# Optimization experiments

Measured on AMD Instinct MI355X. Metric: run time of the kernel, lower is better.

The kernel has to match this reference:

```python
import jax, jax.numpy as jnp
import numpy as np

B, S, V, E, H = 2048, 128, 128, 300, 512  # batch, max_length, vocab, embed, hidden (enc_outstate_dim == H)


def setup_inputs() -> dict:
    key = jax.random.key(0)
    ks = jax.random.split(key, 20)
    s = 0.05
    return {
        "x": jax.random.randint(ks[0], (B, 1), 0, V),
        "hidden": jax.random.normal(ks[1], (1, B, H), jnp.float32),
        "enc_output": jax.random.normal(ks[2], (B, S, H), jnp.float32),
        "emb_table": jax.random.normal(ks[3], (V, E), jnp.float32) * s,
        "W1_w": jax.random.normal(ks[4], (H, H), jnp.float32) * s,
        "W1_b": jnp.zeros((H,), jnp.float32),
        "W2_w": jax.random.normal(ks[5], (H, H), jnp.float32) * s,
        "W2_b": jnp.zeros((H,), jnp.float32),
        "V_w": jax.random.normal(ks[6], (1, H), jnp.float32) * s,
        "V_b": jnp.zeros((1,), jnp.float32),
        "gru_w_ih": jax.random.normal(ks[7], (3 * H, E + H), jnp.float32) * s,
        "gru_w_hh": jax.random.normal(ks[8], (3 * H, H), jnp.float32) * s,
        "gru_b_ih": jnp.zeros((3 * H,), jnp.float32),
        "gru_b_hh": jnp.zeros((3 * H,), jnp.float32),
        "fc1_w": jax.random.normal(ks[9], (E, H), jnp.float32) * s,
        "fc1_b": jnp.zeros((E,), jnp.float32),
        "fc2_w": jax.random.normal(ks[10], (V, E), jnp.float32) * s,
        "fc2_b": jnp.zeros((V,), jnp.float32),
    }


def reference(x, hidden, enc_output, emb_table, W1_w, W1_b, W2_w, W2_b, V_w, V_b,
              gru_w_ih, gru_w_hh, gru_b_ih, gru_b_hh, fc1_w, fc1_b, fc2_w, fc2_b):
    emb = emb_table[x[:, 0]]  # [B,E]
    # Bahdanau additive attention
    hsum = jnp.sum(hidden, axis=0)  # [B,H] (sum over layers)
    score = jnp.tanh(enc_output @ W1_w.T + W1_b + (hsum @ W2_w.T + W2_b)[:, None, :])  # [B,S,H]
    attw = jax.nn.softmax(score @ V_w.T + V_b, axis=1)  # [B,S,1]
    ctx = jnp.sum(attw * enc_output, axis=1)  # [B,H]
    # single-step GRU (PyTorch gate layout: r,z,n)
    gin = jnp.concatenate([ctx, emb], axis=-1)  # [B,H+E]
    h0 = hidden[0]
    gi = gin @ gru_w_ih.T + gru_b_ih
    gh = h0 @ gru_w_hh.T + gru_b_hh
    i_r, i_z, i_n = gi[:, :H], gi[:, H:2 * H], gi[:, 2 * H:]
    h_r, h_z, h_n = gh[:, :H], gh[:, H:2 * H], gh[:, 2 * H:]
    r = jax.nn.sigmoid(i_r + h_r)
    z = jax.nn.sigmoid(i_z + h_z)
    n = jnp.tanh(i_n + r * h_n)
    h_new = (1.0 - z) * n + z * h0  # [B,H]
    # FC head
    y = jax.nn.leaky_relu(h_new @ fc1_w.T + fc1_b, 0.01) @ fc2_w.T + fc2_b  # [B,V]
    return y, h_new[None]
```

## Files before the change

kernel.cpp:

```cpp
#include <hip/hip_runtime.h>


typedef __attribute__((ext_vector_type(4))) float floatx4;
typedef __attribute__((ext_vector_type(8))) short short8;
typedef unsigned short us;

#define DEV static __device__ __forceinline__

DEV us f2bf(float f) {
  unsigned u = __float_as_uint(f);
  u = u + 0x7fffu + ((u >> 16) & 1u);
  return (us)(u >> 16);
}
DEV float bf2f(us s) { return __uint_as_float(((unsigned)s) << 16); }
DEV float tanh_fast(float x) {
  float e = __expf(2.f * x);
  return 1.f - 2.f / (e + 1.f);
}
DEV float sigmoid_fast(float x) { return 1.f / (1.f + __expf(-x)); }
DEV unsigned pack2(float a, float b) {
  return (unsigned)f2bf(a) | ((unsigned)f2bf(b) << 16);
}

#define S0 262144
#define S1 1310720
#define S2 2588672
#define S3 2785280
#define S4 2834432
#define S5 3883008
#define S6 3885056
#define S7 3885440
#define S8 4540800

__global__ void prep_kernel(const float* __restrict__ W1w,
                            const float* __restrict__ W2w,
                            const float* __restrict__ whh,
                            const float* __restrict__ wih,
                            const float* __restrict__ fc1w,
                            const float* __restrict__ fc2w,
                            const float* __restrict__ hidden,
                            const float* __restrict__ W1b,
                            const float* __restrict__ W2b,
                            const float* __restrict__ bhh,
                            const float* __restrict__ fc1b,
                            const int* __restrict__ x,
                            const float* __restrict__ embt,
                            us* __restrict__ W1bf, us* __restrict__ wcomb,
                            us* __restrict__ wihbf, us* __restrict__ fc1wbf,
                            us* __restrict__ fc2wbf, us* __restrict__ hidbf,
                            float* __restrict__ bcomb,
                            float* __restrict__ fc1bp,
                            us* __restrict__ ginbf) {
  int idx = blockIdx.x * 256 + threadIdx.x;
  if (idx < S0) {
    W1bf[idx] = f2bf(W1w[idx]);
  } else if (idx < S1) {
    int i = idx - S0, n = i >> 9, k = i & 511;
    float v = (n < 512) ? W2w[i] : whh[(size_t)(n - 512) * 512 + k];
    wcomb[i] = f2bf(v);
  } else if (idx < S2) {
    int i = idx - S1, n = i / 832, k = i - n * 832;
    wihbf[i] = f2bf(k < 812 ? wih[(size_t)n * 812 + k] : 0.f);
  } else if (idx < S3) {
    int i = idx - S2, n = i >> 9;
    fc1wbf[i] = f2bf(n < 300 ? fc1w[i] : 0.f);
  } else if (idx < S4) {
    int i = idx - S3, n = i / 384, k = i - n * 384;
    fc2wbf[i] = f2bf(k < 300 ? fc2w[(size_t)n * 300 + k] : 0.f);
  } else if (idx < S5) {
    int i = idx - S4;
    hidbf[i] = f2bf(hidden[i]);
  } else if (idx < S6) {
    int i = idx - S5;
    bcomb[i] = (i < 512) ? (W1b[i] + W2b[i]) : bhh[i - 512];
  } else if (idx < S7) {
    int i = idx - S6;
    fc1bp[i] = (i < 300) ? fc1b[i] : 0.f;
  } else if (idx < S8) {
    int i = idx - S7, b = i / 320, e = i - b * 320;
    float v = (e < 300) ? embt[(size_t)x[b] * 300 + e] : 0.f;
    ginbf[(size_t)b * 832 + 512 + e] = f2bf(v);
  }
}

template <int EPI>
__global__ __launch_bounds__(256, 3) void gemm_bt(
    const us* __restrict__ A, int lda, const us* __restrict__ Bm, int ldb,
    const float* __restrict__ bias, void* __restrict__ Cp, int ldc, int K) {
  __shared__ us As[128 * 64];
  __shared__ us Bs[128 * 64];
  int tid = threadIdx.x;
  int bm = blockIdx.x * 128, bn = blockIdx.y * 128;
  int lane = tid & 63, wave = tid >> 6;
  int l15 = lane & 15, l4 = lane >> 4;
  int wm = (wave >> 1) * 64, wn = (wave & 1) * 64;

  floatx4 zero = {0.f, 0.f, 0.f, 0.f};
  floatx4 acc[4][4];
#pragma unroll
  for (int i = 0; i < 4; ++i)
#pragma unroll
    for (int j = 0; j < 4; ++j) acc[i][j] = zero;

  int row = tid >> 1;
  int gc0 = (tid & 1) * 4;
  const us* Aptr = A + (size_t)(bm + row) * lda + gc0 * 8;
  const us* Bptr = Bm + (size_t)(bn + row) * ldb + gc0 * 8;
  int rslot7 = row & 7, lslot7 = l15 & 7;

  uint4 pa[4], pb[4];
#pragma unroll
  for (int i = 0; i < 4; ++i) {
    pa[i] = *(const uint4*)(Aptr + i * 8);
    pb[i] = *(const uint4*)(Bptr + i * 8);
  }

  int nk = K >> 6;
  for (int kt = 0; kt < nk; ++kt) {
    if (kt) __syncthreads();
#pragma unroll
    for (int i = 0; i < 4; ++i) {
      int slot = (gc0 + i) ^ rslot7;
      *(uint4*)&As[row * 64 + slot * 8] = pa[i];
      *(uint4*)&Bs[row * 64 + slot * 8] = pb[i];
    }
    __syncthreads();
    if (kt + 1 < nk) {
#pragma unroll
      for (int i = 0; i < 4; ++i) {
        pa[i] = *(const uint4*)(Aptr + (kt + 1) * 64 + i * 8);
        pb[i] = *(const uint4*)(Bptr + (kt + 1) * 64 + i * 8);
      }
    }
#pragma unroll
    for (int ks = 0; ks < 2; ++ks) {
      int slot = (ks * 4 + l4) ^ lslot7;
      short8 av[4], bv[4];
#pragma unroll
      for (int mt = 0; mt < 4; ++mt)
        av[mt] = *(const short8*)&As[(wm + mt * 16 + l15) * 64 + slot * 8];
#pragma unroll
      for (int nt = 0; nt < 4; ++nt)
        bv[nt] = *(const short8*)&Bs[(wn + nt * 16 + l15) * 64 + slot * 8];
#pragma unroll
      for (int mt = 0; mt < 4; ++mt)
#pragma unroll
        for (int nt = 0; nt < 4; ++nt)
          acc[mt][nt] = __builtin_amdgcn_mfma_f32_16x16x32_bf16(
              av[mt], bv[nt], acc[mt][nt], 0, 0, 0);
    }
  }

#pragma unroll
  for (int nt = 0; nt < 4; ++nt) {
    int n = bn + wn + nt * 16 + l15;
    float bvv = bias[n];
#pragma unroll
    for (int mt = 0; mt < 4; ++mt) {
#pragma unroll
      for (int r = 0; r < 4; ++r) {
        int m = bm + wm + mt * 16 + l4 * 4 + r;
        float v = acc[mt][nt][r] + bvv;
        if (EPI == 1) {
          v = v > 0.f ? v : 0.01f * v;
          ((us*)Cp)[(size_t)m * ldc + n] = f2bf(v);
        } else {
          ((float*)Cp)[(size_t)m * ldc + n] = v;
        }
      }
    }
  }
}

#define ATTN_LDS_BYTES (131072 + 512 + 512 + 2048)

__global__ __launch_bounds__(512, 2) void attn_kernel(
    const float* __restrict__ enc, const us* __restrict__ W1b16,
    const float* __restrict__ keygh, const float* __restrict__ Vw,
    us* __restrict__ gin) {
  extern __shared__ unsigned char smem[];
  us* Albs = (us*)smem;
  float* lds_logits = (float*)(smem + 131072);
  float* lds_attw = lds_logits + 128;
  float* lds_ctx = lds_attw + 128;

  int b = blockIdx.x, tid = threadIdx.x;
  const float* encb = enc + (size_t)b * 65536;
  if (tid < 128) lds_logits[tid] = 0.f;

  int wave = tid >> 6, lane = tid & 63;
  int l15 = lane & 15, l4 = lane >> 4, lslot7 = l15 & 7;
  int n0 = wave * 64;

  int srow = tid >> 2, g0 = tid & 3;
  int c7 = srow & 7;
  int slotA = g0 ^ c7, slotB = (g0 + 4) ^ c7;
  const float* sp = encb + srow * 512 + g0 * 8;
  us* wbase = Albs + srow * 64;

  floatx4 zero = {0.f, 0.f, 0.f, 0.f};
  floatx4 acc[8][4];
#pragma unroll
  for (int i = 0; i < 8; ++i)
#pragma unroll
    for (int j = 0; j < 4; ++j) acc[i][j] = zero;

  float4 p0, p1, p2, p3;
  p0 = *(const float4*)(sp + 0);
  p1 = *(const float4*)(sp + 4);
  p2 = *(const float4*)(sp + 32);
  p3 = *(const float4*)(sp + 36);

  for (int kt = 0; kt < 8; ++kt) {
    uint4 qa, qb;
    qa.x = pack2(p0.x, p0.y); qa.y = pack2(p0.z, p0.w);
    qa.z = pack2(p1.x, p1.y); qa.w = pack2(p1.z, p1.w);
    qb.x = pack2(p2.x, p2.y); qb.y = pack2(p2.z, p2.w);
    qb.z = pack2(p3.x, p3.y); qb.w = pack2(p3.z, p3.w);
    us* wb = wbase + kt * 8192;
    *(uint4*)(wb + slotA * 8) = qa;
    *(uint4*)(wb + slotB * 8) = qb;
    __syncthreads();
    if (kt < 7) {
      const float* np = sp + (kt + 1) * 64;
      p0 = *(const float4*)(np + 0);
      p1 = *(const float4*)(np + 4);
      p2 = *(const float4*)(np + 32);
      p3 = *(const float4*)(np + 36);
    }
#pragma unroll
    for (int ks = 0; ks < 2; ++ks) {
      short8 av[8], bv[4];
#pragma unroll
      for (int nt = 0; nt < 4; ++nt) {
        int n = n0 + nt * 16 + l15;
        bv[nt] = *(const short8*)(W1b16 + (size_t)n * 512 + kt * 64 +
                                  ks * 32 + l4 * 8);
      }
      int slot = (ks * 4 + l4) ^ lslot7;
      const us* rb = Albs + kt * 8192;
#pragma unroll
      for (int mt = 0; mt < 8; ++mt)
        av[mt] = *(const short8*)(rb + (mt * 16 + l15) * 64 + slot * 8);
#pragma unroll
      for (int mt = 0; mt < 8; ++mt)
#pragma unroll
        for (int nt = 0; nt < 4; ++nt)
          acc[mt][nt] = __builtin_amdgcn_mfma_f32_16x16x32_bf16(
              av[mt], bv[nt], acc[mt][nt], 0, 0, 0);
    }
  }

  float kb[4], vwl[4];
#pragma unroll
  for (int nt = 0; nt < 4; ++nt) {
    int col = n0 + nt * 16 + l15;
    kb[nt] = keygh[(size_t)b * 2048 + col];
    vwl[nt] = Vw[col];
  }
#pragma unroll
  for (int mt = 0; mt < 8; ++mt) {
#pragma unroll
    for (int r = 0; r < 4; ++r) {
      float c = 0.f;
#pragma unroll
      for (int nt = 0; nt < 4; ++nt)
        c += tanh_fast(acc[mt][nt][r] + kb[nt]) * vwl[nt];
      c += __shfl_xor(c, 1, 64);
      c += __shfl_xor(c, 2, 64);
      c += __shfl_xor(c, 4, 64);
      c += __shfl_xor(c, 8, 64);
      if (l15 == 0) atomicAdd(&lds_logits[mt * 16 + l4 * 4 + r], c);
    }
  }
  __syncthreads();

  if (wave == 0) {
    float v0 = lds_logits[lane], v1 = lds_logits[lane + 64];
    float mx = fmaxf(v0, v1);
#pragma unroll
    for (int o = 32; o >= 1; o >>= 1) mx = fmaxf(mx, __shfl_xor(mx, o, 64));
    float e0 = __expf(v0 - mx), e1 = __expf(v1 - mx);
    float s = e0 + e1;
#pragma unroll
    for (int o = 32; o >= 1; o >>= 1) s += __shfl_xor(s, o, 64);
    float inv = 1.f / s;
    lds_attw[lane] = e0 * inv;
    lds_attw[lane + 64] = e1 * inv;
  }
  __syncthreads();

  int pr = tid & 255, sh = tid >> 8;
  int h0 = pr * 2;
  int ktc = h0 >> 6, gclc = (h0 & 63) >> 3, dofs = (pr & 3) * 2;
  const us* cb = Albs + ktc * 8192;
  float c0 = 0.f, c1 = 0.f;
  int sbeg = sh * 64;
  for (int s = sbeg; s < sbeg + 64; ++s) {
    int slot = gclc ^ (s & 7);
    unsigned d = *(const unsigned*)(cb + s * 64 + slot * 8 + dofs);
    float aw = lds_attw[s];
    c0 += aw * bf2f((us)(d & 0xffffu));
    c1 += aw * bf2f((us)(d >> 16));
  }
  if (sh == 0) { lds_ctx[h0] = c0; lds_ctx[h0 + 1] = c1; }
  __syncthreads();
  if (sh == 1) {
    unsigned pk = pack2(lds_ctx[h0] + c0, lds_ctx[h0 + 1] + c1);
    *(unsigned*)(gin + (size_t)b * 832 + h0) = pk;
  }
}

__global__ void gru_kernel(const float* __restrict__ gi,
                           const float* __restrict__ keygh,
                           const float* __restrict__ hidden,
                           float* __restrict__ outh,
                           us* __restrict__ hnewbf) {
  int idx = blockIdx.x * 256 + threadIdx.x;
  int b = idx >> 9, h = idx & 511;
  const float* gib = gi + (size_t)b * 1536;
  const float* ghb = keygh + (size_t)b * 2048 + 512;
  float r = sigmoid_fast(gib[h] + ghb[h]);
  float z = sigmoid_fast(gib[512 + h] + ghb[512 + h]);
  float n = tanh_fast(gib[1024 + h] + r * ghb[1024 + h]);
  float h0 = hidden[idx];
  float hn = (1.f - z) * n + z * h0;
  outh[idx] = hn;
  hnewbf[idx] = f2bf(hn);
}

extern "C" void kernel_launch(void* const* d_in, const int* in_sizes, int n_in,
                              void* d_out, int out_size, void* d_ws,
                              size_t ws_size, hipStream_t stream) {
  const int* x = (const int*)d_in[0];
  const float* hidden = (const float*)d_in[1];
  const float* enc = (const float*)d_in[2];
  const float* embt = (const float*)d_in[3];
  const float* W1w = (const float*)d_in[4];
  const float* W1b = (const float*)d_in[5];
  const float* W2w = (const float*)d_in[6];
  const float* W2b = (const float*)d_in[7];
  const float* Vw = (const float*)d_in[8];
  const float* wih = (const float*)d_in[10];
  const float* whh = (const float*)d_in[11];
  const float* bih = (const float*)d_in[12];
  const float* bhh = (const float*)d_in[13];
  const float* fc1w = (const float*)d_in[14];
  const float* fc1b = (const float*)d_in[15];
  const float* fc2w = (const float*)d_in[16];
  const float* fc2b = (const float*)d_in[17];

  float* out_y = (float*)d_out;
  float* out_h = out_y + 2048 * 128;

  char* ws = (char*)d_ws;
  size_t o = 0;
  auto alloc = [&](size_t bytes) {
    size_t r = o;
    o += (bytes + 255) & ~(size_t)255;
    return r;
  };
  us* W1bf   = (us*)(ws + alloc(512 * 512 * 2));
  us* wcomb  = (us*)(ws + alloc(2048 * 512 * 2));
  us* wihbf  = (us*)(ws + alloc(1536 * 832 * 2));
  us* fc1wbf = (us*)(ws + alloc(384 * 512 * 2));
  us* fc2wbf = (us*)(ws + alloc(128 * 384 * 2));
  us* hidbf  = (us*)(ws + alloc(2048 * 512 * 2));
  float* bcomb = (float*)(ws + alloc(2048 * 4));
  float* fc1bp = (float*)(ws + alloc(384 * 4));
  us* ginbf  = (us*)(ws + alloc((size_t)2048 * 832 * 2));
  float* keygh = (float*)(ws + alloc((size_t)2048 * 2048 * 4));
  float* gi    = (float*)(ws + alloc((size_t)2048 * 1536 * 4));
  us* hnewbf = (us*)(ws + alloc(2048 * 512 * 2));
  us* a1bf   = (us*)(ws + alloc((size_t)2048 * 384 * 2));

  prep_kernel<<<(S8 + 255) / 256, 256, 0, stream>>>(
      W1w, W2w, whh, wih, fc1w, fc2w, hidden, W1b, W2b, bhh, fc1b, x, embt,
      W1bf, wcomb, wihbf, fc1wbf, fc2wbf, hidbf, bcomb, fc1bp, ginbf);

  gemm_bt<0><<<dim3(16, 16), 256, 0, stream>>>(hidbf, 512, wcomb, 512, bcomb,
                                               (void*)keygh, 2048, 512);

  (void)hipFuncSetAttribute((const void*)attn_kernel,
                            hipFuncAttributeMaxDynamicSharedMemorySize,
                            ATTN_LDS_BYTES);
  attn_kernel<<<2048, 512, ATTN_LDS_BYTES, stream>>>(enc, W1bf, keygh, Vw,
                                                     ginbf);

  gemm_bt<0><<<dim3(16, 12), 256, 0, stream>>>(ginbf, 832, wihbf, 832, bih,
                                               (void*)gi, 1536, 832);

  gru_kernel<<<2048 * 512 / 256, 256, 0, stream>>>(gi, keygh, hidden, out_h,
                                                   hnewbf);

  gemm_bt<1><<<dim3(16, 3), 256, 0, stream>>>(hnewbf, 512, fc1wbf, 512, fc1bp,
                                              (void*)a1bf, 384, 512);
  gemm_bt<0><<<dim3(16, 1), 256, 0, stream>>>(a1bf, 384, fc2wbf, 384, fc2b,
                                              (void*)out_y, 128, 384);
}
```

Before: 1.039 ms.

## Double attention block to 1024 threads with 32-column wave tiles

The attention kernel now runs 1024 threads (16 waves) per batch row. Each wave computes 32 output columns instead of 64, which halves the accumulator registers. Each thread stages one 8-element chunk of the encoder row per k-step, and the context reduction is split four ways across the sequence and combined through LDS. The aim is more latency hiding and faster staging of the enc tile. In exchange, W1 fragments are loaded more often per block and occupancy is still limited by the 135KB LDS footprint.

```diff
diff --git a/kernel.cpp b/kernel.cpp
--- a/kernel.cpp
+++ b/kernel.cpp
@@ -172,9 +172,9 @@
   }
 }
 
-#define ATTN_LDS_BYTES (131072 + 512 + 512 + 2048)
-
-__global__ __launch_bounds__(512, 2) void attn_kernel(
+#define ATTN_LDS_BYTES (131072 + 512 + 512 + 3 * 512 * 4)
+
+__global__ __launch_bounds__(1024, 4) void attn_kernel(
     const float* __restrict__ enc, const us* __restrict__ W1b16,
     const float* __restrict__ keygh, const float* __restrict__ Vw,
     us* __restrict__ gin) {
@@ -190,70 +190,68 @@
 
   int wave = tid >> 6, lane = tid & 63;
   int l15 = lane & 15, l4 = lane >> 4, lslot7 = l15 & 7;
-  int n0 = wave * 64;
-
-  int srow = tid >> 2, g0 = tid & 3;
-  int c7 = srow & 7;
-  int slotA = g0 ^ c7, slotB = (g0 + 4) ^ c7;
+  int n0 = wave * 32;
+
+  int srow = tid >> 3, g0 = tid & 7;
+  int slotW = g0 ^ (srow & 7);
   const float* sp = encb + srow * 512 + g0 * 8;
-  us* wbase = Albs + srow * 64;
+  us* wbase = Albs + srow * 64 + slotW * 8;
 
   floatx4 zero = {0.f, 0.f, 0.f, 0.f};
-  floatx4 acc[8][4];
-#pragma unroll
-  for (int i = 0; i < 8; ++i)
-#pragma unroll
-    for (int j = 0; j < 4; ++j) acc[i][j] = zero;
-
-  float4 p0, p1, p2, p3;
+  floatx4 acc[8][2];
+#pragma unroll
+  for (int i = 0; i < 8; ++i) {
+    acc[i][0] = zero;
+    acc[i][1] = zero;
+  }
+
+  const us* wptr = W1b16 + (size_t)(n0 + l15) * 512 + l4 * 8;
+
+  float4 p0, p1;
   p0 = *(const float4*)(sp + 0);
   p1 = *(const float4*)(sp + 4);
-  p2 = *(const float4*)(sp + 32);
-  p3 = *(const float4*)(sp + 36);
 
   for (int kt = 0; kt < 8; ++kt) {
-    uint4 qa, qb;
-    qa.x = pack2(p0.x, p0.y); qa.y = pack2(p0.z, p0.w);
-    qa.z = pack2(p1.x, p1.y); qa.w = pack2(p1.z, p1.w);
-    qb.x = pack2(p2.x, p2.y); qb.y = pack2(p2.z, p2.w);
-    qb.z = pack2(p3.x, p3.y); qb.w = pack2(p3.z, p3.w);
-    us* wb = wbase + kt * 8192;
-    *(uint4*)(wb + slotA * 8) = qa;
-    *(uint4*)(wb + slotB * 8) = qb;
+    uint4 q;
+    q.x = pack2(p0.x, p0.y);
+    q.y = pack2(p0.z, p0.w);
+    q.z = pack2(p1.x, p1.y);
+    q.w = pack2(p1.z, p1.w);
+    *(uint4*)(wbase + kt * 8192) = q;
     __syncthreads();
+
+    short8 bv[2][2];
+#pragma unroll
+    for (int ks = 0; ks < 2; ++ks)
+#pragma unroll
+      for (int nt = 0; nt < 2; ++nt)
+        bv[ks][nt] =
+            *(const short8*)(wptr + (size_t)nt * 16 * 512 + kt * 64 + ks * 32);
+
     if (kt < 7) {
       const float* np = sp + (kt + 1) * 64;
       p0 = *(const float4*)(np + 0);
       p1 = *(const float4*)(np + 4);
-      p2 = *(const float4*)(np + 32);
-      p3 = *(const float4*)(np + 36);
-    }
+    }
+
+    const us* rb = Albs + kt * 8192;
 #pragma unroll
     for (int ks = 0; ks < 2; ++ks) {
-      short8 av[8], bv[4];
-#pragma unroll
-      for (int nt = 0; nt < 4; ++nt) {
-        int n = n0 + nt * 16 + l15;
-        bv[nt] = *(const short8*)(W1b16 + (size_t)n * 512 + kt * 64 +
-                                  ks * 32 + l4 * 8);
+      int slot = (ks * 4 + l4) ^ lslot7;
+#pragma unroll
+      for (int mt = 0; mt < 8; ++mt) {
+        short8 av = *(const short8*)(rb + (mt * 16 + l15) * 64 + slot * 8);
+        acc[mt][0] = __builtin_amdgcn_mfma_f32_16x16x32_bf16(
+            av, bv[ks][0], acc[mt][0], 0, 0, 0);
+        acc[mt][1] = __builtin_amdgcn_mfma_f32_16x16x32_bf16(
+            av, bv[ks][1], acc[mt][1], 0, 0, 0);
       }
-      int slot = (ks * 4 + l4) ^ lslot7;
-      const us* rb = Albs + kt * 8192;
-#pragma unroll
-      for (int mt = 0; mt < 8; ++mt)
-        av[mt] = *(const short8*)(rb + (mt * 16 + l15) * 64 + slot * 8);
-#pragma unroll
-      for (int mt = 0; mt < 8; ++mt)
-#pragma unroll
-        for (int nt = 0; nt < 4; ++nt)
-          acc[mt][nt] = __builtin_amdgcn_mfma_f32_16x16x32_bf16(
-              av[mt], bv[nt], acc[mt][nt], 0, 0, 0);
-    }
-  }
-
-  float kb[4], vwl[4];
-#pragma unroll
-  for (int nt = 0; nt < 4; ++nt) {
+    }
+  }
+
+  float kb[2], vwl[2];
+#pragma unroll
+  for (int nt = 0; nt < 2; ++nt) {
     int col = n0 + nt * 16 + l15;
     kb[nt] = keygh[(size_t)b * 2048 + col];
     vwl[nt] = Vw[col];
@@ -262,10 +260,8 @@
   for (int mt = 0; mt < 8; ++mt) {
 #pragma unroll
     for (int r = 0; r < 4; ++r) {
-      float c = 0.f;
-#pragma unroll
-      for (int nt = 0; nt < 4; ++nt)
-        c += tanh_fast(acc[mt][nt][r] + kb[nt]) * vwl[nt];
+      float c = tanh_fast(acc[mt][0][r] + kb[0]) * vwl[0] +
+                tanh_fast(acc[mt][1][r] + kb[1]) * vwl[1];
       c += __shfl_xor(c, 1, 64);
       c += __shfl_xor(c, 2, 64);
       c += __shfl_xor(c, 4, 64);
@@ -292,22 +288,26 @@
 
   int pr = tid & 255, sh = tid >> 8;
   int h0 = pr * 2;
-  int ktc = h0 >> 6, gclc = (h0 & 63) >> 3, dofs = (pr & 3) * 2;
+  int ktc = h0 >> 6, gclc = (h0 & 63) >> 3, dofs = h0 & 7;
   const us* cb = Albs + ktc * 8192;
   float c0 = 0.f, c1 = 0.f;
-  int sbeg = sh * 64;
-  for (int s = sbeg; s < sbeg + 64; ++s) {
+  int sbeg = sh * 32;
+  for (int s = sbeg; s < sbeg + 32; ++s) {
     int slot = gclc ^ (s & 7);
     unsigned d = *(const unsigned*)(cb + s * 64 + slot * 8 + dofs);
     float aw = lds_attw[s];
     c0 += aw * bf2f((us)(d & 0xffffu));
     c1 += aw * bf2f((us)(d >> 16));
   }
-  if (sh == 0) { lds_ctx[h0] = c0; lds_ctx[h0 + 1] = c1; }
+  if (sh != 0) {
+    lds_ctx[(sh - 1) * 512 + h0] = c0;
+    lds_ctx[(sh - 1) * 512 + h0 + 1] = c1;
+  }
   __syncthreads();
-  if (sh == 1) {
-    unsigned pk = pack2(lds_ctx[h0] + c0, lds_ctx[h0 + 1] + c1);
-    *(unsigned*)(gin + (size_t)b * 832 + h0) = pk;
+  if (sh == 0) {
+    c0 += lds_ctx[h0] + lds_ctx[512 + h0] + lds_ctx[1024 + h0];
+    c1 += lds_ctx[h0 + 1] + lds_ctx[512 + h0 + 1] + lds_ctx[1024 + h0 + 1];
+    *(unsigned*)(gin + (size_t)b * 832 + h0) = pack2(c0, c1);
   }
 }
 
@@ -384,8 +384,8 @@
   (void)hipFuncSetAttribute((const void*)attn_kernel,
                             hipFuncAttributeMaxDynamicSharedMemorySize,
                             ATTN_LDS_BYTES);
-  attn_kernel<<<2048, 512, ATTN_LDS_BYTES, stream>>>(enc, W1bf, keygh, Vw,
-                                                     ginbf);
+  attn_kernel<<<2048, 1024, ATTN_LDS_BYTES, stream>>>(enc, W1bf, keygh, Vw,
+                                                      ginbf);
 
   gemm_bt<0><<<dim3(16, 12), 256, 0, stream>>>(ginbf, 832, wihbf, 832, bih,
                                                (void*)gi, 1536, 832);
```

Result: no change. 1.022 ms (-1.7%).
